# Performance work log

Measured on AMD Instinct MI355X. Metric: run time of the kernel, lower is better.

## Reference

```python
import jax, jax.numpy as jnp
import numpy as np

K_TOP = 32
TEMPERATURE = 0.1
EPS = 1e-12  # torch F.normalize eps


def _l2_normalize(x):
    n = jnp.linalg.norm(x, axis=-1, keepdims=True)
    return x / jnp.maximum(n, EPS)


def setup_inputs() -> dict:
    key = jax.random.key(0)
    kq, kk, kv = jax.random.split(key, 3)
    B, T, d_k, d_v, N = 4, 512, 512, 512, 65536
    queries = jax.random.normal(kq, (B, T, d_k), dtype=jnp.float32)
    keys = jax.random.normal(kk, (N, d_k), dtype=jnp.float32)
    values = jax.random.normal(kv, (N, d_v), dtype=jnp.float32)
    return {"queries": queries, "keys": keys, "values": values}


def reference(queries, keys, values):
    B, T, d_k = queries.shape
    d_v = values.shape[1]
    flat_q = queries.reshape(B * T, d_k)
    qn = _l2_normalize(flat_q)           # [BT, d_k]
    kn = _l2_normalize(keys)             # [N, d_k]
    scores = qn @ kn.T                   # [BT, N] cosine similarities
    topk_scores, topk_idx = jax.lax.top_k(scores, K_TOP)  # [BT, K]
    attn = jax.nn.softmax(topk_scores / TEMPERATURE, axis=-1)  # [BT, K]
    retrieved = values[topk_idx]         # [BT, K, d_v]
    aggregated = jnp.einsum('nk,nkd->nd', attn, retrieved)  # [BT, d_v]
    return (aggregated.reshape(B, T, d_v),
            attn.reshape(B, T, K_TOP),
            topk_idx.reshape(B, T, K_TOP))
```

## Files before the change

### kernel.cpp

```cpp
#include <hip/hip_runtime.h>
#include <math.h>

#define M_ROWS 2048
#define N_KEYS 65536
#define DKK 512
#define DVV 512
#define KTOP 32
#define NSPLIT 16
#define NRANGE (N_KEYS / NSPLIT)
#define BM 128
#define BN 128
#define MBLKS (M_ROWS / BM)
#define NTILES (NRANGE / BN)
#define KSTEPS (DKK / 32)
#define TOT (NTILES * KSTEPS)
#define CAP 16
#define CSTR 17
#define TILE_E 4096

typedef _Float16 f16x8 __attribute__((ext_vector_type(8)));
typedef float f32x4 __attribute__((ext_vector_type(4)));


__global__ void __launch_bounds__(256) norm_split_kernel(
    const float* __restrict__ q, const float* __restrict__ keys,
    _Float16* __restrict__ QhT, _Float16* __restrict__ QlT,
    _Float16* __restrict__ KhT, _Float16* __restrict__ KlT) {
  const int gw = (blockIdx.x * 256 + threadIdx.x) >> 6;
  const int lane = threadIdx.x & 63;
  const float* row; _Float16 *oh, *ol; int rr;
  if (gw < M_ROWS) {
    row = q + (size_t)gw * DKK; rr = gw & 127;
    const size_t tb = (size_t)(gw >> 7) * 16 * TILE_E;
    oh = QhT + tb; ol = QlT + tb;
  } else {
    const int n = gw - M_ROWS;
    if (n >= N_KEYS) return;
    row = keys + (size_t)n * DKK; rr = n & 127;
    const size_t tb = (size_t)(n >> 7) * 16 * TILE_E;
    oh = KhT + tb; ol = KlT + tb;
  }
  const float4 a = *(const float4*)&row[lane * 8];
  const float4 b = *(const float4*)&row[lane * 8 + 4];
  float s = a.x*a.x + a.y*a.y + a.z*a.z + a.w*a.w
          + b.x*b.x + b.y*b.y + b.z*b.z + b.w*b.w;
#pragma unroll
  for (int off = 32; off; off >>= 1) s += __shfl_xor(s, off);
  const float inv = 1.0f / fmaxf(sqrtf(s), 1e-12f);

  f16x8 h, l;
  const float e[8] = {a.x, a.y, a.z, a.w, b.x, b.y, b.z, b.w};
#pragma unroll
  for (int j = 0; j < 8; ++j) {
    const float y = e[j] * inv;
    h[j] = (_Float16)y;
    l[j] = (_Float16)(y - (float)h[j]);
  }
  const int ks = lane >> 2, oct = lane & 3;
  const int po = oct ^ ((rr >> 1) & 3);
  const size_t off = (size_t)ks * TILE_E + rr * 32 + po * 8;
  *(f16x8*)&oh[off] = h;
  *(f16x8*)&ol[off] = l;
}

__device__ __forceinline__ void insert32(float* tS, int* tI, float s, int idx) {
  const float ms = tS[31]; const int mi_ = tI[31];
  if (s < ms || (s == ms && idx > mi_)) return;
  int p = 0;
  while (p < KTOP && (tS[p] > s || (tS[p] == s && tI[p] < idx))) ++p;
  for (int qq = KTOP - 1; qq > p; --qq) { tS[qq] = tS[qq-1]; tI[qq] = tI[qq-1]; }
  tS[p] = s; tI[p] = idx;
}

__device__ __forceinline__ void gll16(const _Float16* g, _Float16* l) {
  __builtin_amdgcn_global_load_lds(
      (const __attribute__((address_space(1))) void*)g,
      (__attribute__((address_space(3))) void*)l, 16, 0, 0);
}

__device__ __forceinline__ f16x8 ldsr128(const _Float16* p) {
  f16x8 d;
  const __attribute__((address_space(3))) _Float16* lp =
      (const __attribute__((address_space(3))) _Float16*)p;
  asm volatile("ds_read_b128 %0, %1" : "=v"(d) : "v"(lp));
  return d;
}

#define STAGE(RBS, SG, QKS) do {                                       \
  const size_t _qo = qb + (size_t)(QKS) * TILE_E;                      \
  const size_t _ko = kb0 + (size_t)(SG) * TILE_E;                      \
  gll16(QhT + _qo, &sQh[RBS][ldsA]);                                   \
  gll16(QlT + _qo, &sQl[RBS][ldsA]);                                   \
  gll16(KhT + _ko, &sKh[RBS][ldsA]);                                   \
  gll16(KlT + _ko, &sKl[RBS][ldsA]);                                   \
} while (0)

#define SB0() __builtin_amdgcn_sched_barrier(0)

#define LBAR() do {                                                    \
  SB0(); asm volatile("s_waitcnt lgkmcnt(0)" ::: "memory");            \
  SB0(); __builtin_amdgcn_s_barrier(); SB0();                          \
} while (0)

__global__ void __launch_bounds__(512, 2) gemm_topk_kernel(
    const _Float16* __restrict__ QhT, const _Float16* __restrict__ QlT,
    const _Float16* __restrict__ KhT, const _Float16* __restrict__ KlT,
    float* __restrict__ pscore, int* __restrict__ pidx) {
  __shared__ __attribute__((aligned(16))) _Float16 sQh[3][TILE_E];
  __shared__ __attribute__((aligned(16))) _Float16 sQl[3][TILE_E];
  __shared__ __attribute__((aligned(16))) _Float16 sKh[3][TILE_E];
  __shared__ __attribute__((aligned(16))) _Float16 sKl[3][TILE_E];
  __shared__ float topS[BM * 33];
  __shared__ int   topI[BM * 33];
  __shared__ float candS[BM * CSTR];
  __shared__ int   candI[BM * CSTR];
  __shared__ float mS[BM];
  __shared__ int   cnt[BM];
  __shared__ int   sOver;

  const int tid  = threadIdx.x;
  const int lane = tid & 63;
  const int w    = tid >> 6;
  const int wr   = w >> 1, wc = w & 1;
  const int cl   = lane & 15;
  const int g    = lane >> 4;
  const int g4   = g * 4;

  const int lin   = (int)(blockIdx.x + gridDim.x * blockIdx.y);
  const int virt  = (lin & 7) * 32 + (lin >> 3);
  const int mblk  = virt & (MBLKS - 1);
  const int split = virt >> 4;
  const int qbase  = mblk * BM;
  const int nbase0 = split * NRANGE;

  const int ldsA = tid * 8;
  const size_t qb  = (size_t)mblk * 16 * TILE_E + ldsA;
  const size_t kb0 = (size_t)(split * NTILES) * 16 * TILE_E + ldsA;

  int offA[2], offB[4];
#pragma unroll
  for (int mi = 0; mi < 2; ++mi) {
    const int r = wr * 32 + mi * 16 + cl;
    offA[mi] = r * 32 + (g ^ ((r >> 1) & 3)) * 8;
  }
#pragma unroll
  for (int ni = 0; ni < 4; ++ni) {
    const int c = wc * 64 + ni * 16 + cl;
    offB[ni] = c * 32 + (g ^ ((c >> 1) & 3)) * 8;
  }

  if (tid < BM) {
    mS[tid] = -INFINITY; cnt[tid] = 0;
#pragma unroll
    for (int j = 0; j < KTOP; ++j) { topS[tid*33+j] = -INFINITY; topI[tid*33+j] = 0x7fffffff; }
  }
  if (tid == 0) sOver = 0;

  STAGE(0, 0, 0);
  STAGE(1, 1, 1);

  int rb = 0;

  for (int ct = 0; ct < NTILES; ++ct) {
    const int n0 = nbase0 + ct * BN;
    f32x4 acc[2][4];
#pragma unroll
    for (int mi = 0; mi < 2; ++mi)
#pragma unroll
      for (int ni = 0; ni < 4; ++ni) acc[mi][ni] = (f32x4)0.0f;

    for (int ks = 0; ks < KSTEPS; ++ks) {
      const int s = ct * KSTEPS + ks;
      if (s == TOT - 1) {
        SB0(); asm volatile("s_waitcnt vmcnt(0)" ::: "memory"); SB0();
      } else {
        SB0(); asm volatile("s_waitcnt vmcnt(4)" ::: "memory"); SB0();
      }
      __builtin_amdgcn_s_barrier();
      SB0();

      if (s + 2 < TOT) {
        int rb2 = rb + 2; if (rb2 >= 3) rb2 -= 3;
        STAGE(rb2, s + 2, (s + 2) & 15);
      }
      SB0();

      f16x8 Ah0 = ldsr128(&sQh[rb][offA[0]]);
      f16x8 Ah1 = ldsr128(&sQh[rb][offA[1]]);
      f16x8 Al0 = ldsr128(&sQl[rb][offA[0]]);
      f16x8 Al1 = ldsr128(&sQl[rb][offA[1]]);
      f16x8 Bh[4], Bl[4];
#pragma unroll
      for (int ni = 0; ni < 4; ++ni) {
        Bh[ni] = ldsr128(&sKh[rb][offB[ni]]);
        Bl[ni] = ldsr128(&sKl[rb][offB[ni]]);
      }
      asm volatile("s_waitcnt lgkmcnt(0)" ::: "memory");
      SB0();

      __builtin_amdgcn_s_setprio(1);
#pragma unroll
      for (int ni = 0; ni < 4; ++ni) {
        acc[0][ni] = __builtin_amdgcn_mfma_f32_16x16x32_f16(Al0, Bh[ni], acc[0][ni], 0, 0, 0);
        acc[0][ni] = __builtin_amdgcn_mfma_f32_16x16x32_f16(Ah0, Bl[ni], acc[0][ni], 0, 0, 0);
        acc[0][ni] = __builtin_amdgcn_mfma_f32_16x16x32_f16(Ah0, Bh[ni], acc[0][ni], 0, 0, 0);
        acc[1][ni] = __builtin_amdgcn_mfma_f32_16x16x32_f16(Al1, Bh[ni], acc[1][ni], 0, 0, 0);
        acc[1][ni] = __builtin_amdgcn_mfma_f32_16x16x32_f16(Ah1, Bl[ni], acc[1][ni], 0, 0, 0);
        acc[1][ni] = __builtin_amdgcn_mfma_f32_16x16x32_f16(Ah1, Bh[ni], acc[1][ni], 0, 0, 0);
      }
      __builtin_amdgcn_s_setprio(0);

      ++rb; if (rb >= 3) rb -= 3;
    }

    LBAR();
    float m[2][4];
#pragma unroll
    for (int mi = 0; mi < 2; ++mi) {
      const f32x4 mv = *(const f32x4*)&mS[wr * 32 + mi * 16 + g4];
      m[mi][0] = mv[0]; m[mi][1] = mv[1]; m[mi][2] = mv[2]; m[mi][3] = mv[3];
    }
    unsigned int pend = 0u;
#pragma unroll
    for (int mi = 0; mi < 2; ++mi)
#pragma unroll
      for (int ni = 0; ni < 4; ++ni)
#pragma unroll
        for (int j = 0; j < 4; ++j)
          if (acc[mi][ni][j] >= m[mi][j])
            pend |= 1u << (mi * 16 + ni * 4 + j);

    for (;;) {
      if (pend) {
#pragma unroll
        for (int mi = 0; mi < 2; ++mi)
#pragma unroll
          for (int ni = 0; ni < 4; ++ni)
#pragma unroll
            for (int j = 0; j < 4; ++j) {
              const int bit = mi * 16 + ni * 4 + j;
              if (pend & (1u << bit)) {
                const int r = wr * 32 + mi * 16 + g4 + j;
                const int t = atomicAdd(&cnt[r], 1);
                if (t < CAP) {
                  candS[r * CSTR + t] = acc[mi][ni][j];
                  candI[r * CSTR + t] = n0 + wc * 64 + ni * 16 + cl;
                  pend &= ~(1u << bit);
                }
              }
            }
      }
      LBAR();
      if (tid < BM) {
        int nc = cnt[tid];
        if (nc > CAP) { sOver = 1; nc = CAP; }
        float* tS = &topS[tid * 33];
        int*   tI = &topI[tid * 33];
        for (int e = 0; e < nc; ++e) insert32(tS, tI, candS[tid * CSTR + e], candI[tid * CSTR + e]);
        mS[tid] = tS[KTOP - 1];
        cnt[tid] = 0;
      }
      LBAR();
      const int over = sOver;
      LBAR();
      if (tid == 0) sOver = 0;
      if (!over) break;
#pragma unroll
      for (int mi = 0; mi < 2; ++mi) {
        const f32x4 mv = *(const f32x4*)&mS[wr * 32 + mi * 16 + g4];
        m[mi][0] = mv[0]; m[mi][1] = mv[1]; m[mi][2] = mv[2]; m[mi][3] = mv[3];
      }
      unsigned int keep = 0u;
#pragma unroll
      for (int mi = 0; mi < 2; ++mi)
#pragma unroll
        for (int ni = 0; ni < 4; ++ni)
#pragma unroll
          for (int j = 0; j < 4; ++j) {
            const int bit = mi * 16 + ni * 4 + j;
            if ((pend & (1u << bit)) && acc[mi][ni][j] >= m[mi][j])
              keep |= 1u << bit;
          }
      pend = keep;
    }
  }

  if (tid < BM) {
    const size_t base = ((size_t)(qbase + tid) * NSPLIT + split) * KTOP;
    for (int j = 0; j < KTOP; ++j) {
      pscore[base + j] = topS[tid * 33 + j];
      pidx[base + j]   = topI[tid * 33 + j];
    }
  }
}


#define QB 128
#define NB 128
#define KC 32
#define FNTILES (NRANGE / NB)
#define KCH (DKK / KC)
#define LDST 132

__global__ void __launch_bounds__(256) norm_kernel(
    const float* __restrict__ q, const float* __restrict__ keys,
    float* __restrict__ qn, float* __restrict__ kinv) {
  const int gw = (blockIdx.x * 256 + threadIdx.x) >> 6;
  const int lane = threadIdx.x & 63;
  if (gw < M_ROWS) {
    const float* row = q + (size_t)gw * DKK;
    float4 a = ((const float4*)row)[lane];
    float4 b = ((const float4*)row)[lane + 64];
    float s = a.x*a.x + a.y*a.y + a.z*a.z + a.w*a.w
            + b.x*b.x + b.y*b.y + b.z*b.z + b.w*b.w;
#pragma unroll
    for (int off = 32; off; off >>= 1) s += __shfl_xor(s, off);
    const float inv = 1.0f / fmaxf(sqrtf(s), 1e-12f);
    float* orow = qn + (size_t)gw * DKK;
    ((float4*)orow)[lane]      = make_float4(a.x*inv, a.y*inv, a.z*inv, a.w*inv);
    ((float4*)orow)[lane + 64] = make_float4(b.x*inv, b.y*inv, b.z*inv, b.w*inv);
  } else {
    const int n = gw - M_ROWS;
    if (n < N_KEYS) {
      const float* row = keys + (size_t)n * DKK;
      float4 a = ((const float4*)row)[lane];
      float4 b = ((const float4*)row)[lane + 64];
      float s = a.x*a.x + a.y*a.y + a.z*a.z + a.w*a.w
              + b.x*b.x + b.y*b.y + b.z*b.z + b.w*b.w;
#pragma unroll
      for (int off = 32; off; off >>= 1) s += __shfl_xor(s, off);
      if (lane == 0) kinv[n] = 1.0f / fmaxf(sqrtf(s), 1e-12f);
    }
  }
}

__device__ __forceinline__ void lds_wr_tile(float* dst, int k8, int r, float4 v, float scale) {
  dst[(k8 * 4 + 0) * LDST + r] = v.x * scale;
  dst[(k8 * 4 + 1) * LDST + r] = v.y * scale;
  dst[(k8 * 4 + 2) * LDST + r] = v.z * scale;
  dst[(k8 * 4 + 3) * LDST + r] = v.w * scale;
}

__global__ void __launch_bounds__(256, 1) score_topk_kernel(
    const float* __restrict__ qn, const float* __restrict__ keys,
    const float* __restrict__ kinv,
    float* __restrict__ pscore, int* __restrict__ pidx) {
  __shared__ float u[16896];
  __shared__ float topS[QB * KTOP];
  __shared__ int   topI[QB * KTOP];

  const int tid = threadIdx.x;
  const int tx = tid & 15, ty = tid >> 4;
  const int qbase = blockIdx.y * QB;
  const int nbase0 = blockIdx.x * NRANGE;

  for (int i = tid; i < QB * KTOP; i += 256) { topS[i] = -INFINITY; topI[i] = 0; }
  __syncthreads();

  for (int t = 0; t < FNTILES; ++t) {
    const int n0 = nbase0 + t * NB;
    float acc[8][8];
#pragma unroll
    for (int i = 0; i < 8; ++i)
#pragma unroll
      for (int j = 0; j < 8; ++j) acc[i][j] = 0.0f;

#pragma unroll
    for (int p = 0; p < 4; ++p) {
      const int id = tid + p * 256;
      const int r = id >> 3, k8 = id & 7;
      const float4 va = *(const float4*)&qn[(size_t)(qbase + r) * DKK + k8 * 4];
      const float4 vb = *(const float4*)&keys[(size_t)(n0 + r) * DKK + k8 * 4];
      const float kv = kinv[n0 + r];
      lds_wr_tile(u, k8, r, va, 1.0f);
      lds_wr_tile(u + 4224, k8, r, vb, kv);
    }
    __syncthreads();

    for (int kc = 0; kc < KCH; ++kc) {
      float4 pa[4], pb[4]; float pk[4];
      const bool pre = (kc + 1 < KCH);
      if (pre) {
#pragma unroll
        for (int p = 0; p < 4; ++p) {
          const int id = tid + p * 256;
          const int r = id >> 3, k8 = id & 7;
          pa[p] = *(const float4*)&qn[(size_t)(qbase + r) * DKK + (kc + 1) * KC + k8 * 4];
          pb[p] = *(const float4*)&keys[(size_t)(n0 + r) * DKK + (kc + 1) * KC + k8 * 4];
          pk[p] = kinv[n0 + r];
        }
      }
      const float* As = u + (kc & 1) * 8448;
      const float* Bs = As + 4224;
#pragma unroll 4
      for (int kk = 0; kk < KC; ++kk) {
        const float4 a0 = *(const float4*)&As[kk * LDST + ty * 4];
        const float4 a1 = *(const float4*)&As[kk * LDST + ty * 4 + 64];
        const float4 b0 = *(const float4*)&Bs[kk * LDST + tx * 4];
        const float4 b1 = *(const float4*)&Bs[kk * LDST + tx * 4 + 64];
        const float av[8] = {a0.x,a0.y,a0.z,a0.w,a1.x,a1.y,a1.z,a1.w};
        const float bv[8] = {b0.x,b0.y,b0.z,b0.w,b1.x,b1.y,b1.z,b1.w};
#pragma unroll
        for (int i = 0; i < 8; ++i)
#pragma unroll
          for (int j = 0; j < 8; ++j)
            acc[i][j] = fmaf(av[i], bv[j], acc[i][j]);
      }
      if (pre) {
        float* Ad = u + ((kc + 1) & 1) * 8448;
        float* Bd = Ad + 4224;
#pragma unroll
        for (int p = 0; p < 4; ++p) {
          const int id = tid + p * 256;
          const int r = id >> 3, k8 = id & 7;
          lds_wr_tile(Ad, k8, r, pa[p], 1.0f);
          lds_wr_tile(Bd, k8, r, pb[p], pk[p]);
        }
      }
      __syncthreads();
    }

#pragma unroll
    for (int ib = 0; ib < 2; ++ib)
#pragma unroll
      for (int i = 0; i < 4; ++i) {
        const int r = ty * 4 + i + ib * 64;
#pragma unroll
        for (int jb = 0; jb < 2; ++jb) {
          *(float4*)&u[r * LDST + tx * 4 + jb * 64] =
              make_float4(acc[ib*4+i][jb*4+0], acc[ib*4+i][jb*4+1],
                          acc[ib*4+i][jb*4+2], acc[ib*4+i][jb*4+3]);
        }
      }
    __syncthreads();

    if (tid < QB) {
      const int row = tid;
      float* tS = &topS[row * KTOP];
      int*   tI = &topI[row * KTOP];
      float mSv = tS[KTOP - 1]; int mIv = tI[KTOP - 1];
      for (int c4 = 0; c4 < NB / 4; ++c4) {
        const float4 v = *(const float4*)&u[row * LDST + c4 * 4];
#pragma unroll
        for (int wv = 0; wv < 4; ++wv) {
          const float s = (&v.x)[wv];
          const int idx = n0 + c4 * 4 + wv;
          if (s > mSv || (s == mSv && idx < mIv)) {
            int p = 0;
            while (p < KTOP && (tS[p] > s || (tS[p] == s && tI[p] < idx))) ++p;
            for (int qq = KTOP - 1; qq > p; --qq) { tS[qq] = tS[qq-1]; tI[qq] = tI[qq-1]; }
            tS[p] = s; tI[p] = idx;
            mSv = tS[KTOP - 1]; mIv = tI[KTOP - 1];
          }
        }
      }
    }
    __syncthreads();
  }

  if (tid < QB) {
    const size_t base = ((size_t)(qbase + tid) * NSPLIT + blockIdx.x) * KTOP;
    for (int j = 0; j < KTOP; ++j) {
      pscore[base + j] = topS[tid * KTOP + j];
      pidx[base + j]   = topI[tid * KTOP + j];
    }
  }
}

__global__ void __launch_bounds__(256) merge_kernel(
    const float* __restrict__ pscore, const int* __restrict__ pidx,
    const float* __restrict__ values,
    float* __restrict__ out_agg, float* __restrict__ out_attn, float* __restrict__ out_idx) {
  __shared__ float attn_s[KTOP];
  __shared__ int   sel_i[KTOP];
  const int row = blockIdx.x;
  const int tid = threadIdx.x;

  if (tid < 64) {
    const int lane = tid;
    const float* ps = pscore + (size_t)row * NSPLIT * KTOP;
    const int*   pi = pidx   + (size_t)row * NSPLIT * KTOP;
    int pos = 0;
    float s; int idx;
    if (lane < NSPLIT) { s = ps[lane * KTOP]; idx = pi[lane * KTOP]; }
    else { s = -INFINITY; idx = 0x7fffffff; }
    for (int it = 0; it < KTOP; ++it) {
      float wsv = s; int wi = idx; int wl = lane;
#pragma unroll
      for (int off = 32; off; off >>= 1) {
        const float os = __shfl_xor(wsv, off);
        const int   oi = __shfl_xor(wi, off);
        const int   ol = __shfl_xor(wl, off);
        if (os > wsv || (os == wsv && oi < wi)) { wsv = os; wi = oi; wl = ol; }
      }
      if (lane == 0) { attn_s[it] = wsv; sel_i[it] = wi; }
      if (lane == wl) {
        ++pos;
        if (pos < KTOP) { s = ps[lane * KTOP + pos]; idx = pi[lane * KTOP + pos]; }
        else { s = -INFINITY; idx = 0x7fffffff; }
      }
    }
  }
  __syncthreads();
  if (tid < KTOP) {
    const float mm = attn_s[0];
    const float e = expf((attn_s[tid] - mm) * 10.0f);
    float tsum = e;
#pragma unroll
    for (int off = 16; off; off >>= 1) tsum += __shfl_xor(tsum, off);
    const float a = e / tsum;
    out_attn[(size_t)row * KTOP + tid] = a;
    out_idx [(size_t)row * KTOP + tid] = (float)sel_i[tid];
    attn_s[tid] = a;
  }
  __syncthreads();

  const int d = tid * 2;
  float2 accv = make_float2(0.0f, 0.0f);
  for (int j = 0; j < KTOP; ++j) {
    const float wgt = attn_s[j];
    const float2 v = *(const float2*)&values[(size_t)sel_i[j] * DVV + d];
    accv.x = fmaf(wgt, v.x, accv.x);
    accv.y = fmaf(wgt, v.y, accv.y);
  }
  *(float2*)&out_agg[(size_t)row * DVV + d] = accv;
}

extern "C" void kernel_launch(void* const* d_in, const int* in_sizes, int n_in,
                              void* d_out, int out_size, void* d_ws, size_t ws_size,
                              hipStream_t stream) {
  const float* q      = (const float*)d_in[0];
  const float* keys   = (const float*)d_in[1];
  const float* values = (const float*)d_in[2];

  float* out      = (float*)d_out;
  float* out_agg  = out;
  float* out_attn = out + (size_t)M_ROWS * DVV;
  float* out_idx  = out_attn + (size_t)M_ROWS * KTOP;

  const size_t needFast =
      (size_t)M_ROWS * DKK * 2 * 2
    + (size_t)N_KEYS * DKK * 2 * 2
    + (size_t)M_ROWS * NSPLIT * KTOP * 8;

  if (ws_size >= needFast) {
    _Float16* QhT = (_Float16*)d_ws;
    _Float16* QlT = QhT + (size_t)M_ROWS * DKK;
    _Float16* KhT = QlT + (size_t)M_ROWS * DKK;
    _Float16* KlT = KhT + (size_t)N_KEYS * DKK;
    float* pscore = (float*)(KlT + (size_t)N_KEYS * DKK);
    int*   pidx   = (int*)(pscore + (size_t)M_ROWS * NSPLIT * KTOP);

    norm_split_kernel<<<(M_ROWS + N_KEYS) / 4, 256, 0, stream>>>(q, keys, QhT, QlT, KhT, KlT);
    dim3 g2(MBLKS, NSPLIT, 1);
    gemm_topk_kernel<<<g2, 512, 0, stream>>>(QhT, QlT, KhT, KlT, pscore, pidx);
    merge_kernel<<<M_ROWS, 256, 0, stream>>>(pscore, pidx, values, out_agg, out_attn, out_idx);
  } else {
    float* ws     = (float*)d_ws;
    float* qn     = ws;
    float* kinv   = qn + (size_t)M_ROWS * DKK;
    float* pscore = kinv + N_KEYS;
    int*   pidx   = (int*)(pscore + (size_t)M_ROWS * NSPLIT * KTOP);

    norm_kernel<<<(M_ROWS + N_KEYS) / 4, 256, 0, stream>>>(q, keys, qn, kinv);
    dim3 g2(NSPLIT, M_ROWS / QB, 1);
    score_topk_kernel<<<g2, 256, 0, stream>>>(qn, keys, kinv, pscore, pidx);
    merge_kernel<<<M_ROWS, 256, 0, stream>>>(pscore, pidx, values, out_agg, out_attn, out_idx);
  }
}
```

Baseline: 1.704 ms.

## Screen candidates with fp16-only GEMM, then rescore top-48 exactly in second pass

The main GEMM drops the split-precision hi/lo correction terms and multiplies only the high fp16 halves, cutting its MFMA work to a third and its LDS/global traffic to half. Each split keeps 48 candidates packed as sortable 64-bit score/index keys. A new second pass merges these lists, recomputes the exact scores of the 48 survivors with the full hi/lo products, re-ranks them, and then does the softmax and value aggregation. The N tile is widened to 256. Accuracy now depends on the true top-32 always landing inside the approximate top-48, and the pass-2 global scatter reads add some cost.

```diff
diff --git a/kernel.cpp b/kernel.cpp
--- a/kernel.cpp
+++ b/kernel.cpp
@@ -9,18 +9,32 @@
 #define NSPLIT 16
 #define NRANGE (N_KEYS / NSPLIT)
 #define BM 128
-#define BN 128
+#define BN 256
 #define MBLKS (M_ROWS / BM)
 #define NTILES (NRANGE / BN)
 #define KSTEPS (DKK / 32)
 #define TOT (NTILES * KSTEPS)
-#define CAP 16
-#define CSTR 17
+#define KKEEP 48
+#define KSTR 49
+#define CAP 24
+#define CSTR 25
 #define TILE_E 4096
 
 typedef _Float16 f16x8 __attribute__((ext_vector_type(8)));
 typedef float f32x4 __attribute__((ext_vector_type(4)));
-
+typedef unsigned long long u64t;
+
+
+__device__ __forceinline__ u64t packSI(float s, int idx) {
+  unsigned u = __float_as_uint(s);
+  u = (u & 0x80000000u) ? ~u : (u | 0x80000000u);
+  return ((u64t)u << 32) | (unsigned)(~idx);
+}
+__device__ __forceinline__ float unpackS(u64t p) {
+  unsigned u = (unsigned)(p >> 32);
+  return __uint_as_float((u & 0x80000000u) ? (u ^ 0x80000000u) : ~u);
+}
+#define PNEG_INF ((((u64t)0x007FFFFFu) << 32) | 0x80000000u)
 
 __global__ void __launch_bounds__(256) norm_split_kernel(
     const float* __restrict__ q, const float* __restrict__ keys,
@@ -63,13 +77,12 @@
   *(f16x8*)&ol[off] = l;
 }
 
-__device__ __forceinline__ void insert32(float* tS, int* tI, float s, int idx) {
-  const float ms = tS[31]; const int mi_ = tI[31];
-  if (s < ms || (s == ms && idx > mi_)) return;
+__device__ __forceinline__ void insert48(u64t* tp, u64t v) {
+  if (v <= tp[KKEEP - 1]) return;
   int p = 0;
-  while (p < KTOP && (tS[p] > s || (tS[p] == s && tI[p] < idx))) ++p;
-  for (int qq = KTOP - 1; qq > p; --qq) { tS[qq] = tS[qq-1]; tI[qq] = tI[qq-1]; }
-  tS[p] = s; tI[p] = idx;
+  while (p < KKEEP && tp[p] > v) ++p;
+  for (int qq = KKEEP - 1; qq > p; --qq) tp[qq] = tp[qq - 1];
+  tp[p] = v;
 }
 
 __device__ __forceinline__ void gll16(const _Float16* g, _Float16* l) {
@@ -86,37 +99,30 @@
   return d;
 }
 
-#define STAGE(RBS, SG, QKS) do {                                       \
-  const size_t _qo = qb + (size_t)(QKS) * TILE_E;                      \
-  const size_t _ko = kb0 + (size_t)(SG) * TILE_E;                      \
-  gll16(QhT + _qo, &sQh[RBS][ldsA]);                                   \
-  gll16(QlT + _qo, &sQl[RBS][ldsA]);                                   \
-  gll16(KhT + _ko, &sKh[RBS][ldsA]);                                   \
-  gll16(KlT + _ko, &sKl[RBS][ldsA]);                                   \
-} while (0)
-
 #define SB0() __builtin_amdgcn_sched_barrier(0)
-
 #define LBAR() do {                                                    \
   SB0(); asm volatile("s_waitcnt lgkmcnt(0)" ::: "memory");            \
   SB0(); __builtin_amdgcn_s_barrier(); SB0();                          \
 } while (0)
 
-__global__ void __launch_bounds__(512, 2) gemm_topk_kernel(
-    const _Float16* __restrict__ QhT, const _Float16* __restrict__ QlT,
-    const _Float16* __restrict__ KhT, const _Float16* __restrict__ KlT,
-    float* __restrict__ pscore, int* __restrict__ pidx) {
+#define STAGE(B, S) do {                                               \
+  const int _ct = (S) >> 4, _ks = (S) & 15;                            \
+  gll16(QhT + qtb + (size_t)_ks * TILE_E, &sQh[B][ldsA]);              \
+  const size_t _k0 = ktb + ((size_t)(_ct * 2) * 16 + _ks) * TILE_E;    \
+  gll16(KhT + _k0, &sKh[B][ldsA]);                                     \
+  gll16(KhT + _k0 + 16 * TILE_E, &sKh[B][4096 + ldsA]);                \
+} while (0)
+
+__global__ void __launch_bounds__(512, 2) pass1_kernel(
+    const _Float16* __restrict__ QhT, const _Float16* __restrict__ KhT,
+    u64t* __restrict__ plist) {
   __shared__ __attribute__((aligned(16))) _Float16 sQh[3][TILE_E];
-  __shared__ __attribute__((aligned(16))) _Float16 sQl[3][TILE_E];
-  __shared__ __attribute__((aligned(16))) _Float16 sKh[3][TILE_E];
-  __shared__ __attribute__((aligned(16))) _Float16 sKl[3][TILE_E];
-  __shared__ float topS[BM * 33];
-  __shared__ int   topI[BM * 33];
-  __shared__ float candS[BM * CSTR];
-  __shared__ int   candI[BM * CSTR];
-  __shared__ float mS[BM];
-  __shared__ int   cnt[BM];
-  __shared__ int   sOver;
+  __shared__ __attribute__((aligned(16))) _Float16 sKh[3][2 * TILE_E];
+  __shared__ u64t topP[BM * KSTR];
+  __shared__ u64t candP[BM * CSTR];
+  __shared__ float mSf[BM];
+  __shared__ int cnt[BM];
+  __shared__ int sOver;
 
   const int tid  = threadIdx.x;
   const int lane = tid & 63;
@@ -134,78 +140,69 @@
   const int nbase0 = split * NRANGE;
 
   const int ldsA = tid * 8;
-  const size_t qb  = (size_t)mblk * 16 * TILE_E + ldsA;
-  const size_t kb0 = (size_t)(split * NTILES) * 16 * TILE_E + ldsA;
-
-  int offA[2], offB[4];
+  const size_t qtb = (size_t)mblk * 16 * TILE_E + ldsA;
+  const size_t ktb = (size_t)(split * (NRANGE / 128)) * 16 * TILE_E + ldsA;
+
+  int offA[2], offB[8];
 #pragma unroll
   for (int mi = 0; mi < 2; ++mi) {
     const int r = wr * 32 + mi * 16 + cl;
     offA[mi] = r * 32 + (g ^ ((r >> 1) & 3)) * 8;
   }
 #pragma unroll
-  for (int ni = 0; ni < 4; ++ni) {
-    const int c = wc * 64 + ni * 16 + cl;
-    offB[ni] = c * 32 + (g ^ ((c >> 1) & 3)) * 8;
+  for (int ni = 0; ni < 8; ++ni) {
+    const int c = wc * 128 + ni * 16 + cl;
+    const int crr = c & 127;
+    offB[ni] = (c >> 7) * TILE_E + crr * 32 + (g ^ ((crr >> 1) & 3)) * 8;
   }
 
   if (tid < BM) {
-    mS[tid] = -INFINITY; cnt[tid] = 0;
-#pragma unroll
-    for (int j = 0; j < KTOP; ++j) { topS[tid*33+j] = -INFINITY; topI[tid*33+j] = 0x7fffffff; }
+    mSf[tid] = -INFINITY; cnt[tid] = 0;
+#pragma unroll
+    for (int j = 0; j < KKEEP; ++j) topP[tid * KSTR + j] = PNEG_INF;
   }
   if (tid == 0) sOver = 0;
 
-  STAGE(0, 0, 0);
-  STAGE(1, 1, 1);
-
+  STAGE(0, 0);
+  STAGE(1, 1);
   int rb = 0;
 
   for (int ct = 0; ct < NTILES; ++ct) {
     const int n0 = nbase0 + ct * BN;
-    f32x4 acc[2][4];
+    f32x4 acc[2][8];
 #pragma unroll
     for (int mi = 0; mi < 2; ++mi)
 #pragma unroll
-      for (int ni = 0; ni < 4; ++ni) acc[mi][ni] = (f32x4)0.0f;
+      for (int ni = 0; ni < 8; ++ni) acc[mi][ni] = (f32x4)0.0f;
 
     for (int ks = 0; ks < KSTEPS; ++ks) {
       const int s = ct * KSTEPS + ks;
       if (s == TOT - 1) {
         SB0(); asm volatile("s_waitcnt vmcnt(0)" ::: "memory"); SB0();
       } else {
-        SB0(); asm volatile("s_waitcnt vmcnt(4)" ::: "memory"); SB0();
+        SB0(); asm volatile("s_waitcnt vmcnt(3)" ::: "memory"); SB0();
       }
       __builtin_amdgcn_s_barrier();
       SB0();
 
       if (s + 2 < TOT) {
         int rb2 = rb + 2; if (rb2 >= 3) rb2 -= 3;
-        STAGE(rb2, s + 2, (s + 2) & 15);
+        STAGE(rb2, s + 2);
       }
       SB0();
 
       f16x8 Ah0 = ldsr128(&sQh[rb][offA[0]]);
       f16x8 Ah1 = ldsr128(&sQh[rb][offA[1]]);
-      f16x8 Al0 = ldsr128(&sQl[rb][offA[0]]);
-      f16x8 Al1 = ldsr128(&sQl[rb][offA[1]]);
-      f16x8 Bh[4], Bl[4];
-#pragma unroll
-      for (int ni = 0; ni < 4; ++ni) {
-        Bh[ni] = ldsr128(&sKh[rb][offB[ni]]);
-        Bl[ni] = ldsr128(&sKl[rb][offB[ni]]);
-      }
+      f16x8 Bh[8];
+#pragma unroll
+      for (int ni = 0; ni < 8; ++ni) Bh[ni] = ldsr128(&sKh[rb][offB[ni]]);
       asm volatile("s_waitcnt lgkmcnt(0)" ::: "memory");
       SB0();
 
       __builtin_amdgcn_s_setprio(1);
 #pragma unroll
-      for (int ni = 0; ni < 4; ++ni) {
-        acc[0][ni] = __builtin_amdgcn_mfma_f32_16x16x32_f16(Al0, Bh[ni], acc[0][ni], 0, 0, 0);
-        acc[0][ni] = __builtin_amdgcn_mfma_f32_16x16x32_f16(Ah0, Bl[ni], acc[0][ni], 0, 0, 0);
+      for (int ni = 0; ni < 8; ++ni) {
         acc[0][ni] = __builtin_amdgcn_mfma_f32_16x16x32_f16(Ah0, Bh[ni], acc[0][ni], 0, 0, 0);
-        acc[1][ni] = __builtin_amdgcn_mfma_f32_16x16x32_f16(Al1, Bh[ni], acc[1][ni], 0, 0, 0);
-        acc[1][ni] = __builtin_amdgcn_mfma_f32_16x16x32_f16(Ah1, Bl[ni], acc[1][ni], 0, 0, 0);
         acc[1][ni] = __builtin_amdgcn_mfma_f32_16x16x32_f16(Ah1, Bh[ni], acc[1][ni], 0, 0, 0);
       }
       __builtin_amdgcn_s_setprio(0);
@@ -217,35 +214,34 @@
     float m[2][4];
 #pragma unroll
     for (int mi = 0; mi < 2; ++mi) {
-      const f32x4 mv = *(const f32x4*)&mS[wr * 32 + mi * 16 + g4];
+      const f32x4 mv = *(const f32x4*)&mSf[wr * 32 + mi * 16 + g4];
       m[mi][0] = mv[0]; m[mi][1] = mv[1]; m[mi][2] = mv[2]; m[mi][3] = mv[3];
     }
-    unsigned int pend = 0u;
+    u64t pend = 0ull;
 #pragma unroll
     for (int mi = 0; mi < 2; ++mi)
 #pragma unroll
-      for (int ni = 0; ni < 4; ++ni)
+      for (int ni = 0; ni < 8; ++ni)
 #pragma unroll
         for (int j = 0; j < 4; ++j)
           if (acc[mi][ni][j] >= m[mi][j])
-            pend |= 1u << (mi * 16 + ni * 4 + j);
+            pend |= 1ull << (mi * 32 + ni * 4 + j);
 
     for (;;) {
       if (pend) {
 #pragma unroll
         for (int mi = 0; mi < 2; ++mi)
 #pragma unroll
-          for (int ni = 0; ni < 4; ++ni)
+          for (int ni = 0; ni < 8; ++ni)
 #pragma unroll
             for (int j = 0; j < 4; ++j) {
-              const int bit = mi * 16 + ni * 4 + j;
-              if (pend & (1u << bit)) {
+              const int bit = mi * 32 + ni * 4 + j;
+              if (pend & (1ull << bit)) {
                 const int r = wr * 32 + mi * 16 + g4 + j;
                 const int t = atomicAdd(&cnt[r], 1);
                 if (t < CAP) {
-                  candS[r * CSTR + t] = acc[mi][ni][j];
-                  candI[r * CSTR + t] = n0 + wc * 64 + ni * 16 + cl;
-                  pend &= ~(1u << bit);
+                  candP[r * CSTR + t] = packSI(acc[mi][ni][j], n0 + wc * 128 + ni * 16 + cl);
+                  pend &= ~(1ull << bit);
                 }
               }
             }
@@ -254,10 +250,9 @@
       if (tid < BM) {
         int nc = cnt[tid];
         if (nc > CAP) { sOver = 1; nc = CAP; }
-        float* tS = &topS[tid * 33];
-        int*   tI = &topI[tid * 33];
-        for (int e = 0; e < nc; ++e) insert32(tS, tI, candS[tid * CSTR + e], candI[tid * CSTR + e]);
-        mS[tid] = tS[KTOP - 1];
+        u64t* tp = &topP[tid * KSTR];
+        for (int e = 0; e < nc; ++e) insert48(tp, candP[tid * CSTR + e]);
+        mSf[tid] = unpackS(tp[KKEEP - 1]);
         cnt[tid] = 0;
       }
       LBAR();
@@ -267,31 +262,123 @@
       if (!over) break;
 #pragma unroll
       for (int mi = 0; mi < 2; ++mi) {
-        const f32x4 mv = *(const f32x4*)&mS[wr * 32 + mi * 16 + g4];
+        const f32x4 mv = *(const f32x4*)&mSf[wr * 32 + mi * 16 + g4];
         m[mi][0] = mv[0]; m[mi][1] = mv[1]; m[mi][2] = mv[2]; m[mi][3] = mv[3];
       }
-      unsigned int keep = 0u;
+      u64t keep = 0ull;
 #pragma unroll
       for (int mi = 0; mi < 2; ++mi)
 #pragma unroll
-        for (int ni = 0; ni < 4; ++ni)
+        for (int ni = 0; ni < 8; ++ni)
 #pragma unroll
           for (int j = 0; j < 4; ++j) {
-            const int bit = mi * 16 + ni * 4 + j;
-            if ((pend & (1u << bit)) && acc[mi][ni][j] >= m[mi][j])
-              keep |= 1u << bit;
+            const int bit = mi * 32 + ni * 4 + j;
+            if ((pend & (1ull << bit)) && acc[mi][ni][j] >= m[mi][j])
+              keep |= 1ull << bit;
           }
       pend = keep;
     }
   }
 
   if (tid < BM) {
-    const size_t base = ((size_t)(qbase + tid) * NSPLIT + split) * KTOP;
-    for (int j = 0; j < KTOP; ++j) {
-      pscore[base + j] = topS[tid * 33 + j];
-      pidx[base + j]   = topI[tid * 33 + j];
-    }
-  }
+    u64t* dst = &plist[((size_t)(qbase + tid) * NSPLIT + split) * KKEEP];
+    for (int j = 0; j < KKEEP; ++j) dst[j] = topP[tid * KSTR + j];
+  }
+}
+
+__global__ void __launch_bounds__(256) pass2_kernel(
+    const u64t* __restrict__ plist,
+    const _Float16* __restrict__ QhT, const _Float16* __restrict__ QlT,
+    const _Float16* __restrict__ KhT, const _Float16* __restrict__ KlT,
+    const float* __restrict__ values,
+    float* __restrict__ out_agg, float* __restrict__ out_attn, float* __restrict__ out_idx) {
+  __shared__ u64t sel[KKEEP];
+  __shared__ int selIdx[KKEEP];
+  __shared__ float sEx[KKEEP];
+  __shared__ u64t pEx[KKEEP];
+  __shared__ int sIdx[KKEEP];
+  __shared__ float sSc[KKEEP];
+  __shared__ float attn_s[KTOP];
+
+  const int row = blockIdx.x;
+  const int tid = threadIdx.x;
+  const int lane = tid & 63;
+  const int w = tid >> 6;
+
+  if (tid < 64) {
+    int pos = 0;
+    u64t v = 0;
+    if (lane < NSPLIT) v = plist[((size_t)row * NSPLIT + lane) * KKEEP];
+    for (int it = 0; it < KKEEP; ++it) {
+      u64t wv = v; int wl = lane;
+#pragma unroll
+      for (int off = 32; off; off >>= 1) {
+        const u64t ov = __shfl_xor(wv, off);
+        const int ol = __shfl_xor(wl, off);
+        if (ov > wv) { wv = ov; wl = ol; }
+      }
+      if (lane == 0) sel[it] = wv;
+      if (lane == wl) {
+        ++pos;
+        v = (pos < KKEEP) ? plist[((size_t)row * NSPLIT + lane) * KKEEP + pos] : 0;
+      }
+    }
+  }
+  __syncthreads();
+  if (tid < KKEEP) selIdx[tid] = (int)(~(unsigned)(sel[tid] & 0xffffffffull));
+  __syncthreads();
+
+  if (w < 3) {
+    const int cl = lane & 15, g = lane >> 4;
+    const int c = selIdx[w * 16 + cl];
+    const int crr = c & 127;
+    const int rr = row & 127;
+    const size_t cb  = ((size_t)(c >> 7) * 16) * TILE_E + crr * 32 + (g ^ ((crr >> 1) & 3)) * 8;
+    const size_t qb2 = ((size_t)(row >> 7) * 16) * TILE_E + rr * 32 + (g ^ ((rr >> 1) & 3)) * 8;
+    f32x4 acc = (f32x4)0.0f;
+    for (int ks = 0; ks < KSTEPS; ++ks) {
+      const f16x8 Ah = *(const f16x8*)&QhT[qb2 + (size_t)ks * TILE_E];
+      const f16x8 Al = *(const f16x8*)&QlT[qb2 + (size_t)ks * TILE_E];
+      const f16x8 Bh = *(const f16x8*)&KhT[cb + (size_t)ks * TILE_E];
+      const f16x8 Bl = *(const f16x8*)&KlT[cb + (size_t)ks * TILE_E];
+      acc = __builtin_amdgcn_mfma_f32_16x16x32_f16(Al, Bh, acc, 0, 0, 0);
+      acc = __builtin_amdgcn_mfma_f32_16x16x32_f16(Ah, Bl, acc, 0, 0, 0);
+      acc = __builtin_amdgcn_mfma_f32_16x16x32_f16(Ah, Bh, acc, 0, 0, 0);
+    }
+    if (g == 0) sEx[w * 16 + cl] = acc[0];
+  }
+  __syncthreads();
+  if (tid < KKEEP) pEx[tid] = packSI(sEx[tid], selIdx[tid]);
+  __syncthreads();
+  if (tid < KKEEP) {
+    const u64t me = pEx[tid];
+    int rank = 0;
+    for (int k = 0; k < KKEEP; ++k) rank += (pEx[k] > me);
+    sIdx[rank] = selIdx[tid]; sSc[rank] = sEx[tid];
+  }
+  __syncthreads();
+  if (tid < KTOP) {
+    const float mm = sSc[0];
+    const float e = expf((sSc[tid] - mm) * 10.0f);
+    float tsum = e;
+#pragma unroll
+    for (int off = 16; off; off >>= 1) tsum += __shfl_xor(tsum, off);
+    const float a = e / tsum;
+    out_attn[(size_t)row * KTOP + tid] = a;
+    out_idx [(size_t)row * KTOP + tid] = (float)sIdx[tid];
+    attn_s[tid] = a;
+  }
+  __syncthreads();
+
+  const int d = tid * 2;
+  float2 accv = make_float2(0.0f, 0.0f);
+  for (int j = 0; j < KTOP; ++j) {
+    const float wg = attn_s[j];
+    const float2 v2 = *(const float2*)&values[(size_t)sIdx[j] * DVV + d];
+    accv.x = fmaf(wg, v2.x, accv.x);
+    accv.y = fmaf(wg, v2.y, accv.y);
+  }
+  *(float2*)&out_agg[(size_t)row * DVV + d] = accv;
 }
 
 
@@ -541,20 +628,20 @@
   const size_t needFast =
       (size_t)M_ROWS * DKK * 2 * 2
     + (size_t)N_KEYS * DKK * 2 * 2
-    + (size_t)M_ROWS * NSPLIT * KTOP * 8;
+    + (size_t)M_ROWS * NSPLIT * KKEEP * 8;
 
   if (ws_size >= needFast) {
     _Float16* QhT = (_Float16*)d_ws;
     _Float16* QlT = QhT + (size_t)M_ROWS * DKK;
     _Float16* KhT = QlT + (size_t)M_ROWS * DKK;
     _Float16* KlT = KhT + (size_t)N_KEYS * DKK;
-    float* pscore = (float*)(KlT + (size_t)N_KEYS * DKK);
-    int*   pidx   = (int*)(pscore + (size_t)M_ROWS * NSPLIT * KTOP);
+    u64t* plist   = (u64t*)(KlT + (size_t)N_KEYS * DKK);
 
     norm_split_kernel<<<(M_ROWS + N_KEYS) / 4, 256, 0, stream>>>(q, keys, QhT, QlT, KhT, KlT);
     dim3 g2(MBLKS, NSPLIT, 1);
-    gemm_topk_kernel<<<g2, 512, 0, stream>>>(QhT, QlT, KhT, KlT, pscore, pidx);
-    merge_kernel<<<M_ROWS, 256, 0, stream>>>(pscore, pidx, values, out_agg, out_attn, out_idx);
+    pass1_kernel<<<g2, 512, 0, stream>>>(QhT, KhT, plist);
+    pass2_kernel<<<M_ROWS, 256, 0, stream>>>(plist, QhT, QlT, KhT, KlT, values,
+                                             out_agg, out_attn, out_idx);
   } else {
     float* ws     = (float*)d_ws;
     float* qn     = ws;
```

New measurement: 2.723 ms. +59.8%, slower.
